# Performance work log

Measured on AMD Instinct MI355X. Metric: run time of the kernel, lower is better.

The kernel has to match this reference:

```python
import jax, jax.numpy as jnp
import numpy as np

NUM_HEADS = 12
THETA = 10000.0


def _rope(x, pos):
    # x: [B, H, S, dk]; interleaved even/odd pair rotation
    dk = x.shape[-1]
    freqs = THETA ** (-jnp.arange(dk // 2, dtype=jnp.float32) * 2.0 / dk)  # [dk/2]
    ang = pos.astype(jnp.float32)[:, None] * freqs                         # [S, dk/2]
    cos, sin = jnp.cos(ang), jnp.sin(ang)
    x1, x2 = x[..., 0::2], x[..., 1::2]
    rot = jnp.stack([x1 * cos - x2 * sin, x1 * sin + x2 * cos], axis=-1)
    return rot.reshape(x.shape)


def setup_inputs() -> dict:
    key = jax.random.key(0)
    ks = jax.random.split(key, 5)
    B, S, D = 4, 2048, 768
    w_scale = 1.0 / np.sqrt(D).astype(np.float32)
    x = jax.random.normal(ks[0], (B, S, D), dtype=jnp.float32)
    Wq = jax.random.normal(ks[1], (D, D), dtype=jnp.float32) * w_scale
    Wk = jax.random.normal(ks[2], (D, D), dtype=jnp.float32) * w_scale
    Wv = jax.random.normal(ks[3], (D, D), dtype=jnp.float32) * w_scale
    Wo = jax.random.normal(ks[4], (D, D), dtype=jnp.float32) * w_scale
    token_positions = jnp.arange(S, dtype=jnp.int32)
    return {"x": x, "Wq": Wq, "Wk": Wk, "Wv": Wv, "Wo": Wo,
            "token_positions": token_positions}


def reference(x, Wq, Wk, Wv, Wo, token_positions):
    B, S, D = x.shape
    H = NUM_HEADS
    dk = D // H
    # bias-free linear layers: y = x @ W^T (torch Linear weight convention)
    q = (x @ Wq.T).reshape(B, S, H, dk).transpose(0, 2, 1, 3)  # [B,H,S,dk]
    k = (x @ Wk.T).reshape(B, S, H, dk).transpose(0, 2, 1, 3)
    v = (x @ Wv.T).reshape(B, S, H, dk).transpose(0, 2, 1, 3)
    q = _rope(q, token_positions)
    k = _rope(k, token_positions)
    scores = jnp.einsum('bhqd,bhkd->bhqk', q, k) / np.float32(np.sqrt(dk))
    causal = jnp.tril(jnp.ones((S, S), dtype=bool))
    scores = jnp.where(causal, scores, -jnp.inf)
    attn = jax.nn.softmax(scores, axis=-1)                      # [B,H,S,S]
    out = jnp.einsum('bhqk,bhkd->bhqd', attn, v)
    out = out.transpose(0, 2, 1, 3).reshape(B, S, D)
    return out @ Wo.T
```

## Files before the change

kernel.cpp:

```cpp
#include <hip/hip_runtime.h>
#include <cstdint>
#include <cstddef>

#define NTOK 8192
#define SLEN 2048
#define DM   768
#define NH   12
#define DKH  64

typedef __attribute__((ext_vector_type(8))) short bf16x8;
typedef __attribute__((ext_vector_type(4))) float f32x4;

__device__ __forceinline__ float b2f(unsigned short u) {
  return __uint_as_float(((unsigned)u) << 16);
}
__device__ __forceinline__ unsigned short f2b(float f) {
  unsigned u = __float_as_uint(f);
  u += 0x7fffu + ((u >> 16) & 1u);
  return (unsigned short)(u >> 16);
}
__device__ __forceinline__ unsigned cvtpk(float lo, float hi) {
  unsigned r;
  asm("v_cvt_pk_bf16_f32 %0, %1, %2" : "=v"(r) : "v"(lo), "v"(hi));
  return r;
}

__device__ __forceinline__ void gld16(const void* g, void* l) {
  __builtin_amdgcn_global_load_lds(
      (const __attribute__((address_space(1))) void*)g,
      (__attribute__((address_space(3))) void*)l, 16, 0, 0);
}

#define BAR_DRAIN() do {                                  \
    asm volatile("s_waitcnt vmcnt(0)" ::: "memory");      \
    __builtin_amdgcn_s_barrier();                         \
    __builtin_amdgcn_sched_barrier(0);                    \
  } while (0)

__global__ void cast_all_kernel(const float* __restrict__ x,
                                const float* __restrict__ w0,
                                const float* __restrict__ w1,
                                const float* __restrict__ w2,
                                const float* __restrict__ w3,
                                unsigned short* __restrict__ xb,
                                unsigned short* __restrict__ wb) {
  const int bid = blockIdx.x, tid = threadIdx.x;
  const float* src;
  unsigned short* dst;
  size_t i;
  if (bid < 3072) {
    src = x; dst = xb; i = (size_t)bid * 256 + tid;
  } else {
    const int wbid = bid - 3072;
    const int w = wbid / 288;
    src = (w == 0) ? w0 : (w == 1) ? w1 : (w == 2) ? w2 : w3;
    dst = wb + (size_t)w * DM * DM;
    i = (size_t)(wbid - w * 288) * 256 + tid;
  }
  const float4* p = (const float4*)(src + i * 8);
  float4 a = p[0], b = p[1];
  union { unsigned short h[8]; bf16x8 v; } u;
  u.h[0] = f2b(a.x); u.h[1] = f2b(a.y); u.h[2] = f2b(a.z); u.h[3] = f2b(a.w);
  u.h[4] = f2b(b.x); u.h[5] = f2b(b.y); u.h[6] = f2b(b.z); u.h[7] = f2b(b.w);
  *(bf16x8*)(dst + i * 8) = u.v;
}

__global__ __launch_bounds__(256, 4) void gemm_qkv_kernel(
    const unsigned short* __restrict__ A, const unsigned short* __restrict__ Ball,
    unsigned short* __restrict__ Qb, unsigned short* __restrict__ Kb,
    unsigned short* __restrict__ VTout,
    const int* __restrict__ pos) {
  const int K = DM;
  const int tid = threadIdx.x, wid = tid >> 6, lane = tid & 63;
  const int lrow = lane & 15, g = lane >> 4, lk8 = g * 8;
  const int m0 = blockIdx.y * 64, n0 = blockIdx.x * 128;
  const int wm = (wid >> 1) * 32, wn = (wid & 1) * 64;
  const int sr = wid * 8 + (lane >> 3), sc = (lane & 7) * 8;
  const int ssw = sc ^ ((sr & 7) << 3);
  __shared__ unsigned short At[64 * 64];
  __shared__ unsigned short Bt[128 * 64];
  f32x4 acc[2][4] = {};

  const unsigned short* ap = A    + (size_t)(m0 + sr) * K + ssw;
  const unsigned short* bp = Ball + (size_t)(n0 + sr) * K + ssw;

  int aoff[2][2], boff[2][4];
#pragma unroll
  for (int ks = 0; ks < 2; ++ks) {
#pragma unroll
    for (int mi = 0; mi < 2; ++mi) {
      int ra = wm + mi * 16 + lrow;
      aoff[ks][mi] = (ra * 64 + ((ks * 32 + lk8) ^ ((ra & 7) << 3))) * 2;
    }
#pragma unroll
    for (int ni = 0; ni < 4; ++ni) {
      int rb = wn + ni * 16 + lrow;
      boff[ks][ni] = (rb * 64 + ((ks * 32 + lk8) ^ ((rb & 7) << 3))) * 2;
    }
  }
  const char* Atc = (const char*)At;
  const char* Btc = (const char*)Bt;

  const int nk = K >> 6;
  for (int kk = 0; kk < nk; ++kk) {
    __syncthreads();
    gld16(ap,          &At[(wid * 8) * 64]);
    gld16(ap + 32 * K, &At[(32 + wid * 8) * 64]);
#pragma unroll
    for (int rnd = 0; rnd < 4; ++rnd)
      gld16(bp + rnd * 32 * K, &Bt[(rnd * 32 + wid * 8) * 64]);
    ap += 64; bp += 64;
    __syncthreads();
    bf16x8 af[2][2], bfr[2][4];
#pragma unroll
    for (int ks = 0; ks < 2; ++ks) {
#pragma unroll
      for (int mi = 0; mi < 2; ++mi)
        af[ks][mi] = *(const bf16x8*)(Atc + aoff[ks][mi]);
#pragma unroll
      for (int ni = 0; ni < 4; ++ni)
        bfr[ks][ni] = *(const bf16x8*)(Btc + boff[ks][ni]);
    }
#pragma unroll
    for (int ks = 0; ks < 2; ++ks)
#pragma unroll
      for (int mi = 0; mi < 2; ++mi)
#pragma unroll
        for (int ni = 0; ni < 4; ++ni)
          acc[mi][ni] = __builtin_amdgcn_mfma_f32_16x16x32_bf16(
              bfr[ks][ni], af[ks][mi], acc[mi][ni], 0, 0, 0);
  }

  const int nsec = blockIdx.x / 6;
  const int nn0 = n0 - nsec * 768;

  if (nsec == 2) {
#pragma unroll
    for (int mi = 0; mi < 2; ++mi) {
      const int m = m0 + wm + mi * 16 + lrow;
      const int bb = m >> 11, st = m & (SLEN - 1);
      const int scol = (st & ~63) | (st & 35) |
                       (((st >> 4) & 1) << 2) | (((st >> 2) & 1) << 3) |
                       (((st >> 3) & 1) << 4);
#pragma unroll
      for (int ni = 0; ni < 4; ++ni) {
        const int nb = nn0 + wn + ni * 16 + g * 4;
        const int hh = nb >> 6, dd = nb & 63;
        unsigned short* dst =
            VTout + ((size_t)(bb * NH + hh) * DKH + dd) * SLEN + scol;
#pragma unroll
        for (int r = 0; r < 4; ++r)
          dst[(size_t)r * SLEN] = f2b(acc[mi][ni][r]);
      }
    }
    return;
  }

  unsigned short* Cp = (nsec == 0) ? Qb : Kb;
  float frq[4][2];
#pragma unroll
  for (int ni = 0; ni < 4; ++ni)
#pragma unroll
    for (int rp = 0; rp < 2; ++rp)
      frq[ni][rp] = exp2f(
          (float)(((wn + ni * 16 + g * 4 + rp * 2) & 63) >> 1) *
          -0.4152410118609203f);
#pragma unroll
  for (int mi = 0; mi < 2; ++mi) {
    const int m = m0 + wm + mi * 16 + lrow;
    const float ps = (float)pos[m & (SLEN - 1)];
#pragma unroll
    for (int ni = 0; ni < 4; ++ni) {
#pragma unroll
      for (int rp = 0; rp < 2; ++rp) {
        float sn, cs;
        __sincosf(ps * frq[ni][rp], &sn, &cs);
        float x1 = acc[mi][ni][2 * rp], x2 = acc[mi][ni][2 * rp + 1];
        acc[mi][ni][2 * rp]     = fmaf(x1, cs, -x2 * sn);
        acc[mi][ni][2 * rp + 1] = fmaf(x1, sn, x2 * cs);
      }
      union { unsigned u[2]; ushort4 s; } o;
      o.u[0] = cvtpk(acc[mi][ni][0], acc[mi][ni][1]);
      o.u[1] = cvtpk(acc[mi][ni][2], acc[mi][ni][3]);
      *(ushort4*)&Cp[(size_t)m * DM + nn0 + wn + ni * 16 + g * 4] = o.s;
    }
  }
}

__global__ __launch_bounds__(256, 4) void gemm_out_kernel(
    const unsigned short* __restrict__ A, const unsigned short* __restrict__ B,
    float* __restrict__ C) {
  const int K = DM, N = DM;
  const int tid = threadIdx.x, wid = tid >> 6, lane = tid & 63;
  const int lrow = lane & 15, g = lane >> 4, lk8 = g * 8;
  const int m0 = blockIdx.y * 64, n0 = blockIdx.x * 128;
  const int wm = (wid >> 1) * 32, wn = (wid & 1) * 64;
  const int sr = wid * 8 + (lane >> 3), sc = (lane & 7) * 8;
  const int ssw = sc ^ ((sr & 7) << 3);
  __shared__ unsigned short At[64 * 64];
  __shared__ unsigned short Bt[128 * 64];
  f32x4 acc[2][4] = {};

  const unsigned short* ap = A + (size_t)(m0 + sr) * K + ssw;
  const unsigned short* bp = B + (size_t)(n0 + sr) * K + ssw;

  int aoff[2][2], boff[2][4];
#pragma unroll
  for (int ks = 0; ks < 2; ++ks) {
#pragma unroll
    for (int mi = 0; mi < 2; ++mi) {
      int ra = wm + mi * 16 + lrow;
      aoff[ks][mi] = (ra * 64 + ((ks * 32 + lk8) ^ ((ra & 7) << 3))) * 2;
    }
#pragma unroll
    for (int ni = 0; ni < 4; ++ni) {
      int rb = wn + ni * 16 + lrow;
      boff[ks][ni] = (rb * 64 + ((ks * 32 + lk8) ^ ((rb & 7) << 3))) * 2;
    }
  }
  const char* Atc = (const char*)At;
  const char* Btc = (const char*)Bt;

  const int nk = K >> 6;
  for (int kk = 0; kk < nk; ++kk) {
    __syncthreads();
    gld16(ap,          &At[(wid * 8) * 64]);
    gld16(ap + 32 * K, &At[(32 + wid * 8) * 64]);
#pragma unroll
    for (int rnd = 0; rnd < 4; ++rnd)
      gld16(bp + rnd * 32 * K, &Bt[(rnd * 32 + wid * 8) * 64]);
    ap += 64; bp += 64;
    __syncthreads();
    bf16x8 af[2][2], bfr[2][4];
#pragma unroll
    for (int ks = 0; ks < 2; ++ks) {
#pragma unroll
      for (int mi = 0; mi < 2; ++mi)
        af[ks][mi] = *(const bf16x8*)(Atc + aoff[ks][mi]);
#pragma unroll
      for (int ni = 0; ni < 4; ++ni)
        bfr[ks][ni] = *(const bf16x8*)(Btc + boff[ks][ni]);
    }
#pragma unroll
    for (int ks = 0; ks < 2; ++ks)
#pragma unroll
      for (int mi = 0; mi < 2; ++mi)
#pragma unroll
        for (int ni = 0; ni < 4; ++ni)
          acc[mi][ni] = __builtin_amdgcn_mfma_f32_16x16x32_bf16(
              bfr[ks][ni], af[ks][mi], acc[mi][ni], 0, 0, 0);
  }

#pragma unroll
  for (int mi = 0; mi < 2; ++mi) {
    const int m = m0 + wm + mi * 16 + lrow;
#pragma unroll
    for (int ni = 0; ni < 4; ++ni)
      *(f32x4*)&C[(size_t)m * N + n0 + wn + ni * 16 + g * 4] = acc[mi][ni];
  }
}

__global__ __launch_bounds__(256, 5) void attn_kernel(
    const unsigned short* __restrict__ Q, const unsigned short* __restrict__ Kg,
    const unsigned short* __restrict__ VT, unsigned short* __restrict__ O) {
  const int bh = blockIdx.x;
  const int s = 31 - (int)blockIdx.y;
  const int nt = s + 1;
  const int b = bh / NH, h = bh - b * NH;
  const size_t base = ((size_t)b * SLEN) * DM + h * DKH;
  const size_t vbase = (size_t)bh * DKH * SLEN;
  const int tid = threadIdx.x, wid = tid >> 6, lane = tid & 63;
  const int lrow = lane & 15, g = lane >> 4;
  const int rloc = wid * 16 + lrow;

  __shared__ unsigned short Kt[2][64 * 64];
  __shared__ unsigned short Vt[2][64 * 64];

  bf16x8 qf[2];
#pragma unroll
  for (int ks = 0; ks < 2; ++ks) {
    union { unsigned short h[8]; bf16x8 v; } u;
    u.v = *(const bf16x8*)&Q[base + (size_t)(s * 64 + rloc) * DM + ks * 32 + g * 8];
#pragma unroll
    for (int j = 0; j < 8; ++j)
      u.h[j] = f2b(b2f(u.h[j]) * 0.18033688011112042f);
    qf[ks] = u.v;
  }

  union { unsigned short h[8]; bf16x8 v; } one_u;
#pragma unroll
  for (int j = 0; j < 8; ++j) one_u.h[j] = 0x3F80;
  const bf16x8 ones = one_u.v;

  f32x4 oacc[4] = {};
  f32x4 l_acc = {};

  const int srow = wid * 8 + (lane >> 3);
  const int ssw = ((lane & 7) * 8) ^ ((srow & 7) << 3);
  const unsigned short* kp = Kg + base + (size_t)srow * DM + ssw;
  const unsigned short* vp = VT + vbase + (size_t)srow * SLEN + ssw;

  int roff[2][4];
#pragma unroll
  for (int ks = 0; ks < 2; ++ks)
#pragma unroll
    for (int ni = 0; ni < 4; ++ni) {
      int rr = ni * 16 + lrow;
      roff[ks][ni] = (rr * 64 + ((ks * 32 + g * 8) ^ ((rr & 7) << 3))) * 2;
    }

  auto stage = [&](int buf) {
    gld16(kp,             &Kt[buf][(wid * 8) * 64]);
    gld16(kp + 32 * DM,   &Kt[buf][(32 + wid * 8) * 64]);
    gld16(vp,             &Vt[buf][(wid * 8) * 64]);
    gld16(vp + 32 * SLEN, &Vt[buf][(32 + wid * 8) * 64]);
    kp += 64 * DM;
    vp += 64;
  };

  auto compute = [&](int t, int buf) {
    const char* Ksb = (const char*)&Kt[buf][0];
    const char* Vsb = (const char*)&Vt[buf][0];

    f32x4 sa[4] = {};
    __builtin_amdgcn_s_setprio(1);
#pragma unroll
    for (int ks = 0; ks < 2; ++ks)
#pragma unroll
      for (int ni = 0; ni < 4; ++ni) {
        bf16x8 kf = *(const bf16x8*)(Ksb + roff[ks][ni]);
        sa[ni] = __builtin_amdgcn_mfma_f32_16x16x32_bf16(
            kf, qf[ks], sa[ni], 0, 0, 0);
      }
    __builtin_amdgcn_s_setprio(0);

    if (t == s) {
#pragma unroll
      for (int ni = 0; ni < 4; ++ni)
#pragma unroll
        for (int r = 0; r < 4; ++r)
          if (ni * 16 + g * 4 + r > rloc) sa[ni][r] = -1e30f;
    }

#pragma unroll
    for (int ni = 0; ni < 4; ++ni)
#pragma unroll
      for (int r = 0; r < 4; ++r)
        sa[ni][r] = exp2f(sa[ni][r]);

    bf16x8 pf[2];
#pragma unroll
    for (int ks = 0; ks < 2; ++ks) {
      union { unsigned u[4]; bf16x8 v; } uu;
      uu.u[0] = cvtpk(sa[2 * ks][0],     sa[2 * ks][1]);
      uu.u[1] = cvtpk(sa[2 * ks][2],     sa[2 * ks][3]);
      uu.u[2] = cvtpk(sa[2 * ks + 1][0], sa[2 * ks + 1][1]);
      uu.u[3] = cvtpk(sa[2 * ks + 1][2], sa[2 * ks + 1][3]);
      pf[ks] = uu.v;
    }

    __builtin_amdgcn_s_setprio(1);
#pragma unroll
    for (int ks = 0; ks < 2; ++ks) {
#pragma unroll
      for (int ni = 0; ni < 4; ++ni) {
        bf16x8 vf = *(const bf16x8*)(Vsb + roff[ks][ni]);
        oacc[ni] = __builtin_amdgcn_mfma_f32_16x16x32_bf16(
            vf, pf[ks], oacc[ni], 0, 0, 0);
      }
      l_acc = __builtin_amdgcn_mfma_f32_16x16x32_bf16(
          ones, pf[ks], l_acc, 0, 0, 0);
    }
    __builtin_amdgcn_s_setprio(0);
  };

  stage(0);
  BAR_DRAIN();
  int cur = 0;
  for (int t = 0; t < nt; ++t) {
    if (t + 1 < nt) stage(cur ^ 1);
    compute(t, cur);
    BAR_DRAIN();
    cur ^= 1;
  }

  const float inv = 1.f / l_acc[0];
  const int qrow = s * 64 + rloc;
#pragma unroll
  for (int ni = 0; ni < 4; ++ni) {
    union { unsigned u[2]; ushort4 s4; } o;
    o.u[0] = cvtpk(oacc[ni][0] * inv, oacc[ni][1] * inv);
    o.u[1] = cvtpk(oacc[ni][2] * inv, oacc[ni][3] * inv);
    *(ushort4*)&O[base + (size_t)qrow * DM + ni * 16 + g * 4] = o.s4;
  }
}

extern "C" void kernel_launch(void* const* d_in, const int* in_sizes, int n_in,
                              void* d_out, int out_size, void* d_ws, size_t ws_size,
                              hipStream_t stream) {
  const float* x  = (const float*)d_in[0];
  const float* Wq = (const float*)d_in[1];
  const float* Wk = (const float*)d_in[2];
  const float* Wv = (const float*)d_in[3];
  const float* Wo = (const float*)d_in[4];
  const int* pos  = (const int*)d_in[5];
  float* out = (float*)d_out;

  char* ws = (char*)d_ws;
  size_t off = 0;
  auto carve = [&](size_t bytes) -> void* {
    void* p = ws + off;
    off += (bytes + 255) & ~(size_t)255;
    return p;
  };
  unsigned short* xb  = (unsigned short*)carve((size_t)NTOK * DM * 2);
  unsigned short* wqb = (unsigned short*)carve((size_t)DM * DM * 2 * 4);
  unsigned short* wob = wqb + (size_t)3 * DM * DM;
  unsigned short* Qb  = (unsigned short*)carve((size_t)NTOK * DM * 2);
  unsigned short* Kb  = (unsigned short*)carve((size_t)NTOK * DM * 2);
  unsigned short* Ab  = (unsigned short*)carve((size_t)NTOK * DM * 2);
  unsigned short* VTb = (unsigned short*)carve((size_t)4 * NH * DKH * SLEN * 2);

  cast_all_kernel<<<dim3(3072 + 4 * 288), dim3(256), 0, stream>>>(
      x, Wq, Wk, Wv, Wo, xb, wqb);

  gemm_qkv_kernel<<<dim3(18, 128), dim3(256), 0, stream>>>(
      xb, wqb, Qb, Kb, VTb, pos);

  attn_kernel<<<dim3(48, 32), dim3(256), 0, stream>>>(Qb, Kb, VTb, Ab);

  gemm_out_kernel<<<dim3(6, 128), dim3(256), 0, stream>>>(Ab, wob, out);
}
```

Measured before the change: 117.6 us.

## Widen attention blocks to 128 query rows sharing each staged K/V tile

The attention kernel now runs 512-thread blocks that cover 128 query rows (8 waves), so each K/V tile staged into shared memory serves twice as many queries and global K/V traffic per query halves. Each thread issues one async load per tensor instead of two, and the grid shrinks to 16 query tiles per head. On the last key tile the first four waves skip compute, and masking is generalized to a per-wave diagonal check. The tradeoff is fewer blocks, more idle waves at the diagonal, and higher register pressure under the new launch bounds.

```diff
diff --git a/kernel.cpp b/kernel.cpp
--- a/kernel.cpp
+++ b/kernel.cpp
@@ -260,18 +260,18 @@
   }
 }
 
-__global__ __launch_bounds__(256, 5) void attn_kernel(
+__global__ __launch_bounds__(512, 6) void attn_kernel(
     const unsigned short* __restrict__ Q, const unsigned short* __restrict__ Kg,
     const unsigned short* __restrict__ VT, unsigned short* __restrict__ O) {
   const int bh = blockIdx.x;
-  const int s = 31 - (int)blockIdx.y;
-  const int nt = s + 1;
+  const int qt = 15 - (int)blockIdx.y;
+  const int nkt = 2 * qt + 2;
   const int b = bh / NH, h = bh - b * NH;
   const size_t base = ((size_t)b * SLEN) * DM + h * DKH;
   const size_t vbase = (size_t)bh * DKH * SLEN;
   const int tid = threadIdx.x, wid = tid >> 6, lane = tid & 63;
   const int lrow = lane & 15, g = lane >> 4;
-  const int rloc = wid * 16 + lrow;
+  const int qg = qt * 128 + wid * 16 + lrow;
 
   __shared__ unsigned short Kt[2][64 * 64];
   __shared__ unsigned short Vt[2][64 * 64];
@@ -280,7 +280,7 @@
 #pragma unroll
   for (int ks = 0; ks < 2; ++ks) {
     union { unsigned short h[8]; bf16x8 v; } u;
-    u.v = *(const bf16x8*)&Q[base + (size_t)(s * 64 + rloc) * DM + ks * 32 + g * 8];
+    u.v = *(const bf16x8*)&Q[base + (size_t)qg * DM + ks * 32 + g * 8];
 #pragma unroll
     for (int j = 0; j < 8; ++j)
       u.h[j] = f2b(b2f(u.h[j]) * 0.18033688011112042f);
@@ -295,8 +295,8 @@
   f32x4 oacc[4] = {};
   f32x4 l_acc = {};
 
-  const int srow = wid * 8 + (lane >> 3);
-  const int ssw = ((lane & 7) * 8) ^ ((srow & 7) << 3);
+  const int srow = tid >> 3;
+  const int ssw = ((tid & 7) * 8) ^ ((srow & 7) << 3);
   const unsigned short* kp = Kg + base + (size_t)srow * DM + ssw;
   const unsigned short* vp = VT + vbase + (size_t)srow * SLEN + ssw;
 
@@ -310,15 +310,14 @@
     }
 
   auto stage = [&](int buf) {
-    gld16(kp,             &Kt[buf][(wid * 8) * 64]);
-    gld16(kp + 32 * DM,   &Kt[buf][(32 + wid * 8) * 64]);
-    gld16(vp,             &Vt[buf][(wid * 8) * 64]);
-    gld16(vp + 32 * SLEN, &Vt[buf][(32 + wid * 8) * 64]);
+    gld16(kp, &Kt[buf][(wid * 8) * 64]);
+    gld16(vp, &Vt[buf][(wid * 8) * 64]);
     kp += 64 * DM;
     vp += 64;
   };
 
-  auto compute = [&](int t, int buf) {
+  auto compute = [&](int kt, int buf) {
+    if (kt == 2 * qt + 1 && wid < 4) return;
     const char* Ksb = (const char*)&Kt[buf][0];
     const char* Vsb = (const char*)&Vt[buf][0];
 
@@ -334,12 +333,13 @@
       }
     __builtin_amdgcn_s_setprio(0);
 
-    if (t == s) {
+    if (kt * 64 + 64 > qt * 128 + wid * 16) {
+      const int kb = kt * 64 + g * 4;
 #pragma unroll
       for (int ni = 0; ni < 4; ++ni)
 #pragma unroll
         for (int r = 0; r < 4; ++r)
-          if (ni * 16 + g * 4 + r > rloc) sa[ni][r] = -1e30f;
+          if (kb + ni * 16 + r > qg) sa[ni][r] = -1e30f;
     }
 
 #pragma unroll
@@ -377,21 +377,20 @@
   stage(0);
   BAR_DRAIN();
   int cur = 0;
-  for (int t = 0; t < nt; ++t) {
-    if (t + 1 < nt) stage(cur ^ 1);
-    compute(t, cur);
+  for (int kt = 0; kt < nkt; ++kt) {
+    if (kt + 1 < nkt) stage(cur ^ 1);
+    compute(kt, cur);
     BAR_DRAIN();
     cur ^= 1;
   }
 
   const float inv = 1.f / l_acc[0];
-  const int qrow = s * 64 + rloc;
 #pragma unroll
   for (int ni = 0; ni < 4; ++ni) {
     union { unsigned u[2]; ushort4 s4; } o;
     o.u[0] = cvtpk(oacc[ni][0] * inv, oacc[ni][1] * inv);
     o.u[1] = cvtpk(oacc[ni][2] * inv, oacc[ni][3] * inv);
-    *(ushort4*)&O[base + (size_t)qrow * DM + ni * 16 + g * 4] = o.s4;
+    *(ushort4*)&O[base + (size_t)qg * DM + ni * 16 + g * 4] = o.s4;
   }
 }
 
@@ -427,7 +426,7 @@
   gemm_qkv_kernel<<<dim3(18, 128), dim3(256), 0, stream>>>(
       xb, wqb, Qb, Kb, VTb, pos);
 
-  attn_kernel<<<dim3(48, 32), dim3(256), 0, stream>>>(Qb, Kb, VTb, Ab);
+  attn_kernel<<<dim3(48, 16), dim3(512), 0, stream>>>(Qb, Kb, VTb, Ab);
 
   gemm_out_kernel<<<dim3(6, 128), dim3(256), 0, stream>>>(Ab, wob, out);
 }
```

Measured after the change: 120.5 us. 1.02x slower.
